# Kernel optimization log

Hardware: AMD Instinct MI355X
Metric: run time of the kernel (lower is better)

## Reference

```python
import jax, jax.numpy as jnp
import numpy as np

N = 8192
IN_F = 256
HEADS = 4
HF = 64            # head_features = out_features / heads
OUT_F = HEADS * HF # concat=True
NEG_SLOPE = 0.2


def setup_inputs() -> dict:
    key = jax.random.key(0)
    ks = jax.random.split(key, 7)
    x = jax.random.normal(ks[0], (N, IN_F), dtype=jnp.float32)
    graph = jax.random.randint(ks[1], (N, N), 0, 2, dtype=jnp.int32)
    weight = jax.random.normal(ks[2], (HEADS, IN_F, HF), dtype=jnp.float32) * (1.0 / np.sqrt(IN_F))
    weight_i = jax.random.normal(ks[3], (HEADS, HF, 1), dtype=jnp.float32) * (1.0 / np.sqrt(HF))
    weight_j = jax.random.normal(ks[4], (HEADS, HF, 1), dtype=jnp.float32) * (1.0 / np.sqrt(HF))
    weight_r = jax.random.normal(ks[5], (IN_F, HF * HEADS), dtype=jnp.float32) * (1.0 / np.sqrt(IN_F))
    bias = jnp.zeros((OUT_F,), dtype=jnp.float32)
    return {"x": x, "graph": graph, "weight": weight, "weight_i": weight_i,
            "weight_j": weight_j, "weight_r": weight_r, "bias": bias}


def reference(x, graph, weight, weight_i, weight_j, weight_r, bias):
    # h: per-head projected features [heads, N, hf]
    h = jnp.einsum('nm,hmf->hnf', x, weight)
    # additive attention logits: coe_i [h,N,1] + coe_j [h,1,N]
    coe_i = jnp.einsum('hnf,hfo->hno', h, weight_i)          # [heads, N, 1]
    coe_j = jnp.einsum('hnf,hfo->hno', h, weight_j)          # [heads, N, 1]
    coe = jax.nn.leaky_relu(coe_i + jnp.swapaxes(coe_j, 1, 2), NEG_SLOPE)  # [heads, N, N]
    # adjacency mask (note transpose, matching the torch code)
    mask = jnp.where(graph > 0, 0.0, -jnp.inf).T             # [N, N]
    att = jax.nn.softmax(coe + mask[None], axis=-1)          # [heads, N, N]
    # aggregate and move heads to axis 1: [N, heads, hf]
    y = jnp.einsum('hij,hjf->ihf', att, h)
    # residual with projection (in_features != head_features)
    y = y + (x @ weight_r).reshape(N, HEADS, HF)
    # concat heads + bias
    y = y.reshape(N, OUT_F) + bias
    return y
```

## Files before the change

kernel.cpp:

```cpp
#include <hip/hip_runtime.h>
#include <hip/hip_bf16.h>

#define N 8192
#define IN_F 256
#define HEADS 4
#define HF 64
#define OUT_F 256

typedef __attribute__((ext_vector_type(8))) short short8;
typedef __attribute__((ext_vector_type(4))) float f32x4;

__device__ __forceinline__ float lrelu(float x) {
    return fmaxf(x, 0.0f) * 0.8f + x * 0.2f;
}
__device__ __forceinline__ short f2bf(float f) {
    union { __hip_bfloat16 h; short s; } u;
    u.h = __float2bfloat16(f);
    return u.s;
}
__device__ __forceinline__ float bf2f(unsigned short b) {
    union { unsigned u; float f; } v; v.u = ((unsigned)b) << 16;
    return v.f;
}
__device__ __forceinline__ unsigned pack_bf16(float p0, float p1) {
    union { __hip_bfloat162 b; unsigned u; } cv;
    cv.b = __float22bfloat162_rn(make_float2(p0, p1));
    return cv.u;
}

__global__ __launch_bounds__(256) void k_wcvt(
    const float* __restrict__ w, const float* __restrict__ wr,
    unsigned short* __restrict__ BbT)
{
    int c = blockIdx.x;
    int k = threadIdx.x;
    float v;
    if (c < 256) {
        int head = c >> 6, f = c & 63;
        v = w[((size_t)head * IN_F + k) * HF + f];
    } else {
        v = wr[(size_t)k * OUT_F + (c - 256)];
    }
    BbT[(size_t)c * IN_F + k] = (unsigned short)f2bf(v);
}

__global__ __launch_bounds__(256) void k_gemm_pack(
    const float* __restrict__ x, const unsigned short* __restrict__ BbT,
    const float* __restrict__ bias,
    unsigned short* __restrict__ hT, float* __restrict__ out,
    const int* __restrict__ graph, unsigned int* __restrict__ bits)
{
    __shared__ unsigned short Asw[64 * 64];
    __shared__ unsigned short Bsw[128 * 64];
    int b = blockIdx.x;
    int t = threadIdx.x;

    if (b >= 512) {
        int p = b - 512;
        int jw = p & 255;
        int i = (p >> 8) * 256 + t;
        const int* gp = graph + (size_t)(jw * 32) * N + i;
        unsigned int word = 0;
        #pragma unroll
        for (int k = 0; k < 32; ++k)
            word |= (gp[(size_t)k * N] > 0 ? 1u : 0u) << k;
        bits[(size_t)jw * N + i] = word;
        return;
    }

    int m0 = (b & 127) * 64;
    int bn = b >> 7;
    int w_ = t >> 6, l = t & 63;
    int wr_ = w_ >> 1, wc_ = w_ & 1;
    int ar = l & 15, g = l >> 4;

    f32x4 acc[2][4];
    #pragma unroll
    for (int m = 0; m < 2; ++m)
        #pragma unroll
        for (int n = 0; n < 4; ++n) acc[m][n] = (f32x4){0.f, 0.f, 0.f, 0.f};

    int srow = t >> 2, skq = (t & 3) * 16;
    int sc = t >> 1, sh = (t & 1) * 32;

    for (int kt = 0; kt < 4; ++kt) {
        const float* xs = x + (size_t)(m0 + srow) * IN_F + kt * 64 + skq;
        float4 xa = ((const float4*)xs)[0];
        float4 xb = ((const float4*)xs)[1];
        float4 xc = ((const float4*)xs)[2];
        float4 xd = ((const float4*)xs)[3];
        unsigned ae[8];
        ae[0] = pack_bf16(xa.x, xa.y); ae[1] = pack_bf16(xa.z, xa.w);
        ae[2] = pack_bf16(xb.x, xb.y); ae[3] = pack_bf16(xb.z, xb.w);
        ae[4] = pack_bf16(xc.x, xc.y); ae[5] = pack_bf16(xc.z, xc.w);
        ae[6] = pack_bf16(xd.x, xd.y); ae[7] = pack_bf16(xd.z, xd.w);
        int kb0 = (skq >> 3) ^ (srow & 7);
        int kb1 = ((skq >> 3) + 1) ^ (srow & 7);
        *(uint4*)&Asw[srow * 64 + kb0 * 8] = *(uint4*)&ae[0];
        *(uint4*)&Asw[srow * 64 + kb1 * 8] = *(uint4*)&ae[4];
        const unsigned short* bs = BbT + (size_t)(bn * 128 + sc) * IN_F + kt * 64 + sh;
        uint4 b0 = ((const uint4*)bs)[0];
        uint4 b1 = ((const uint4*)bs)[1];
        uint4 b2 = ((const uint4*)bs)[2];
        uint4 b3 = ((const uint4*)bs)[3];
        int hb = sh >> 3;
        *(uint4*)&Bsw[sc * 64 + ((hb + 0) ^ (sc & 7)) * 8] = b0;
        *(uint4*)&Bsw[sc * 64 + ((hb + 1) ^ (sc & 7)) * 8] = b1;
        *(uint4*)&Bsw[sc * 64 + ((hb + 2) ^ (sc & 7)) * 8] = b2;
        *(uint4*)&Bsw[sc * 64 + ((hb + 3) ^ (sc & 7)) * 8] = b3;
        __syncthreads();
        #pragma unroll
        for (int ks = 0; ks < 2; ++ks) {
            short8 af[2], bf[4];
            #pragma unroll
            for (int m = 0; m < 2; ++m) {
                int row = wr_ * 32 + m * 16 + ar;
                int kb = (ks * 4 + g) ^ (row & 7);
                af[m] = *(const short8*)&Asw[row * 64 + kb * 8];
            }
            #pragma unroll
            for (int n = 0; n < 4; ++n) {
                int c = wc_ * 64 + n * 16 + ar;
                int kb = (ks * 4 + g) ^ (c & 7);
                bf[n] = *(const short8*)&Bsw[c * 64 + kb * 8];
            }
            #pragma unroll
            for (int m = 0; m < 2; ++m)
                #pragma unroll
                for (int n = 0; n < 4; ++n)
                    acc[m][n] = __builtin_amdgcn_mfma_f32_16x16x32_bf16(af[m], bf[n], acc[m][n], 0, 0, 0);
        }
        __syncthreads();
    }
    #pragma unroll
    for (int m = 0; m < 2; ++m) {
        #pragma unroll
        for (int n = 0; n < 4; ++n) {
            int cg = bn * 128 + wc_ * 64 + n * 16 + ar;
            int mg0 = m0 + wr_ * 32 + m * 16 + g * 4;
            if (cg < 256) {
                int head = cg >> 6, f = cg & 63;
                unsigned pk[2];
                pk[0] = pack_bf16(acc[m][n][0], acc[m][n][1]);
                pk[1] = pack_bf16(acc[m][n][2], acc[m][n][3]);
                *(uint2*)(hT + (size_t)(head * HF + f) * N + mg0) = *(uint2*)pk;
            } else {
                float bb = bias[cg - 256];
                #pragma unroll
                for (int r = 0; r < 4; ++r)
                    out[(size_t)(mg0 + r) * OUT_F + (cg - 256)] = acc[m][n][r] + bb;
            }
        }
    }
}

__global__ __launch_bounds__(256) void k_coe(
    const unsigned short* __restrict__ hT, const float* __restrict__ wi,
    const float* __restrict__ wj, float* __restrict__ coe_i, float* __restrict__ coe_j)
{
    int head = blockIdx.y;
    int n = blockIdx.x * 256 + threadIdx.x;
    const unsigned short* hp = hT + (size_t)head * HF * N + n;
    float si = 0.f, sj = 0.f;
    #pragma unroll 8
    for (int f = 0; f < HF; ++f) {
        float hv = bf2f(hp[(size_t)f * N]);
        si = fmaf(hv, wi[head * HF + f], si);
        sj = fmaf(hv, wj[head * HF + f], sj);
    }
    coe_i[head * N + n] = si;
    coe_j[head * N + n] = sj;
}

__global__ __launch_bounds__(256) void k_cols(
    const float* __restrict__ coe_j, float* __restrict__ maxB,
    float* __restrict__ F, float* __restrict__ H)
{
    __shared__ float red[256];
    int head = blockIdx.x;
    int t = threadIdx.x;
    float m = -1e30f;
    for (int n = t; n < N; n += 256) {
        float b = coe_j[head * N + n];
        F[head * N + n] = __expf(b);
        H[head * N + n] = __expf(0.2f * b);
        m = fmaxf(m, b);
    }
    red[t] = m;
    __syncthreads();
    for (int s = 128; s > 0; s >>= 1) {
        if (t < s) red[t] = fmaxf(red[t], red[t + s]);
        __syncthreads();
    }
    if (t == 0) maxB[head] = red[0];
}

__device__ __forceinline__ short8 makeP(
    const float4& fa, const float4& fb4, const float4& ha, const float4& hb4,
    unsigned int mk, float Ei, float Gi)
{
    float fv[8] = {fa.x, fa.y, fa.z, fa.w, fb4.x, fb4.y, fb4.z, fb4.w};
    float hv[8] = {ha.x, ha.y, ha.z, ha.w, hb4.x, hb4.y, hb4.z, hb4.w};
    union { short8 s8; unsigned u[4]; } A;
    #pragma unroll
    for (int jp = 0; jp < 4; ++jp) {
        float p0 = fmaxf(Ei * fv[2 * jp],     Gi * hv[2 * jp]);
        float p1 = fmaxf(Ei * fv[2 * jp + 1], Gi * hv[2 * jp + 1]);
        int s0 = __builtin_amdgcn_sbfe((int)mk, 2 * jp, 1);
        int s1 = __builtin_amdgcn_sbfe((int)mk, 2 * jp + 1, 1);
        p0 = __int_as_float(__float_as_int(p0) & s0);
        p1 = __int_as_float(__float_as_int(p1) & s1);
        A.u[jp] = pack_bf16(p0, p1);
    }
    return A.s8;
}

__global__ __launch_bounds__(512) void k_att(
    const unsigned short* __restrict__ hT, const float* __restrict__ coe_i,
    const float* __restrict__ maxB, const float* __restrict__ F,
    const float* __restrict__ H, const unsigned int* __restrict__ bits,
    float* __restrict__ out)
{
    __shared__ char smem[65536];
    unsigned short* hb = (unsigned short*)smem;
    float* mbuf = (float*)smem;

    int t = threadIdx.x;
    int head = blockIdx.y;
    int i0 = blockIdx.x * 64;
    int w = t >> 6, l = t & 63;
    int rg = w >> 2, grp = w & 3;
    int ar = l & 15, g = l >> 4, g8 = g * 8;

    int irow0 = i0 + rg * 32 + ar;
    int irow1 = irow0 + 16;
    float mB = maxB[head];
    float a0 = coe_i[head * N + irow0];
    float a1 = coe_i[head * N + irow1];
    float M0 = lrelu(a0 + mB);
    float M1 = lrelu(a1 + mB);
    float Ei0 = __expf(a0 - M0), Gi0 = __expf(0.2f * a0 - M0);
    float Ei1 = __expf(a1 - M1), Gi1 = __expf(0.2f * a1 - M1);

    f32x4 acc0[4], acc1[4];
    #pragma unroll
    for (int fb = 0; fb < 4; ++fb) {
        acc0[fb] = (f32x4){0.f, 0.f, 0.f, 0.f};
        acc1[fb] = (f32x4){0.f, 0.f, 0.f, 0.f};
    }
    f32x4 accd0 = (f32x4){0.f, 0.f, 0.f, 0.f};
    f32x4 accd1 = (f32x4){0.f, 0.f, 0.f, 0.f};

    short8 ones;
    #pragma unroll
    for (int k = 0; k < 8; ++k) ones[k] = (short)0x3F80;

    int grp_s = t >> 7;
    int v = t & 127;
    int sf = v >> 1;
    int gsel = v & 1;
    const unsigned short* hsrc = hT + ((size_t)(head * HF + sf) * N) + grp_s * 64 + gsel * 32;
    int sfk = sf & 7;
    int wbase = grp_s * 4096 + sf * 64;
    int pgA = ((gsel * 4 + 0) ^ sfk) * 8;
    int pgB = ((gsel * 4 + 1) ^ sfk) * 8;
    int pgC = ((gsel * 4 + 2) ^ sfk) * 8;
    int pgD = ((gsel * 4 + 3) ^ sfk) * 8;

    const float* Fp = F + head * N + g8;
    const float* Hp = H + head * N + g8;
    const unsigned int* bp0 = bits + irow0;
    const unsigned int* bp1 = bits + irow1;

    uint4 hv0 = *(const uint4*)(hsrc + 0);
    uint4 hv1 = *(const uint4*)(hsrc + 8);
    uint4 hv2 = *(const uint4*)(hsrc + 16);
    uint4 hv3 = *(const uint4*)(hsrc + 24);
    int jt0 = grp * 64;
    size_t jw0 = (size_t)(jt0 >> 5);
    unsigned int mk00 = bp0[jw0 * N] >> g8;
    unsigned int mk01 = bp0[(jw0 + 1) * N] >> g8;
    unsigned int mk10 = bp1[jw0 * N] >> g8;
    unsigned int mk11 = bp1[(jw0 + 1) * N] >> g8;

    for (int s = 0; s < 32; ++s) {
        int jt = s * 256 + grp * 64;
        float4 fa0 = *(const float4*)(Fp + jt);
        float4 fb0 = *(const float4*)(Fp + jt + 4);
        float4 ha0 = *(const float4*)(Hp + jt);
        float4 hb0 = *(const float4*)(Hp + jt + 4);
        float4 fa1 = *(const float4*)(Fp + jt + 32);
        float4 fb1 = *(const float4*)(Fp + jt + 36);
        float4 ha1 = *(const float4*)(Hp + jt + 32);
        float4 hb1 = *(const float4*)(Hp + jt + 36);
        int bo = (s & 1) * 16384;
        *(uint4*)&hb[bo + wbase + pgA] = hv0;
        *(uint4*)&hb[bo + wbase + pgB] = hv1;
        *(uint4*)&hb[bo + wbase + pgC] = hv2;
        *(uint4*)&hb[bo + wbase + pgD] = hv3;
        int sn = (s + 1 < 32) ? s + 1 : s;
        const unsigned short* hn = hsrc + (size_t)sn * 256;
        hv0 = *(const uint4*)(hn + 0);
        hv1 = *(const uint4*)(hn + 8);
        hv2 = *(const uint4*)(hn + 16);
        hv3 = *(const uint4*)(hn + 24);
        int jtn = sn * 256 + grp * 64;
        size_t jwn = (size_t)(jtn >> 5);
        unsigned int nk00 = bp0[jwn * N] >> g8;
        unsigned int nk01 = bp0[(jwn + 1) * N] >> g8;
        unsigned int nk10 = bp1[jwn * N] >> g8;
        unsigned int nk11 = bp1[(jwn + 1) * N] >> g8;
        short8 af00 = makeP(fa0, fb0, ha0, hb0, mk00, Ei0, Gi0);
        short8 af10 = makeP(fa0, fb0, ha0, hb0, mk10, Ei1, Gi1);
        short8 af01 = makeP(fa1, fb1, ha1, hb1, mk01, Ei0, Gi0);
        short8 af11 = makeP(fa1, fb1, ha1, hb1, mk11, Ei1, Gi1);
        asm volatile("s_waitcnt lgkmcnt(0)" ::: "memory");
        __builtin_amdgcn_s_barrier();
        __builtin_amdgcn_sched_barrier(0);
        const unsigned short* rb = &hb[bo + grp * 4096];
        #pragma unroll
        for (int ss = 0; ss < 2; ++ss) {
            short8 a0f = ss ? af01 : af00;
            short8 a1f = ss ? af11 : af10;
            #pragma unroll
            for (int fb = 0; fb < 4; ++fb) {
                int row = fb * 16 + ar;
                int pg = (ss * 4 + g) ^ (ar & 7);
                short8 bfr = *(const short8*)&rb[row * 64 + pg * 8];
                acc0[fb] = __builtin_amdgcn_mfma_f32_16x16x32_bf16(a0f, bfr, acc0[fb], 0, 0, 0);
                acc1[fb] = __builtin_amdgcn_mfma_f32_16x16x32_bf16(a1f, bfr, acc1[fb], 0, 0, 0);
            }
            accd0 = __builtin_amdgcn_mfma_f32_16x16x32_bf16(a0f, ones, accd0, 0, 0, 0);
            accd1 = __builtin_amdgcn_mfma_f32_16x16x32_bf16(a1f, ones, accd1, 0, 0, 0);
        }
        mk00 = nk00; mk01 = nk01; mk10 = nk10; mk11 = nk11;
    }

    __syncthreads();
    int slot = rg * 64 + l;
    if (grp > 0) {
        float* dst = mbuf + (size_t)(grp - 1) * 5248 + slot * 41;
        #pragma unroll
        for (int fb = 0; fb < 4; ++fb)
            #pragma unroll
            for (int r = 0; r < 4; ++r) {
                dst[fb * 4 + r] = acc0[fb][r];
                dst[16 + fb * 4 + r] = acc1[fb][r];
            }
        #pragma unroll
        for (int r = 0; r < 4; ++r) {
            dst[32 + r] = accd0[r];
            dst[36 + r] = accd1[r];
        }
    }
    __syncthreads();
    if (grp == 0) {
        #pragma unroll
        for (int q = 0; q < 3; ++q) {
            const float* src = mbuf + (size_t)q * 5248 + slot * 41;
            #pragma unroll
            for (int fb = 0; fb < 4; ++fb)
                #pragma unroll
                for (int r = 0; r < 4; ++r) {
                    acc0[fb][r] += src[fb * 4 + r];
                    acc1[fb][r] += src[16 + fb * 4 + r];
                }
            #pragma unroll
            for (int r = 0; r < 4; ++r) {
                accd0[r] += src[32 + r];
                accd1[r] += src[36 + r];
            }
        }
        #pragma unroll
        for (int r = 0; r < 4; ++r) {
            float inv0 = 1.0f / accd0[r];
            float inv1 = 1.0f / accd1[r];
            int orow0 = i0 + rg * 32 + g * 4 + r;
            float* op0 = out + (size_t)orow0 * OUT_F + head * HF + ar;
            float* op1 = op0 + 16 * OUT_F;
            #pragma unroll
            for (int fb = 0; fb < 4; ++fb) {
                op0[fb * 16] += acc0[fb][r] * inv0;
                op1[fb * 16] += acc1[fb][r] * inv1;
            }
        }
    }
}

extern "C" void kernel_launch(void* const* d_in, const int* in_sizes, int n_in,
                              void* d_out, int out_size, void* d_ws, size_t ws_size,
                              hipStream_t stream) {
    const float* x     = (const float*)d_in[0];
    const int*   graph = (const int*)d_in[1];
    const float* w     = (const float*)d_in[2];
    const float* wi    = (const float*)d_in[3];
    const float* wj    = (const float*)d_in[4];
    const float* wr    = (const float*)d_in[5];
    const float* bias  = (const float*)d_in[6];
    float* out = (float*)d_out;

    char* ws = (char*)d_ws;
    unsigned short* hT  = (unsigned short*)(ws);
    float* coe_i = (float*)(ws + 4194304);
    float* coe_j = (float*)(ws + 4325376);
    float* maxB  = (float*)(ws + 4456448);
    float* F     = (float*)(ws + 4457472);
    float* H     = (float*)(ws + 4588544);
    unsigned short* BbT = (unsigned short*)(ws + 4719616);
    unsigned int* bits  = (unsigned int*)(ws + 4981760);

    k_wcvt<<<dim3(512), 256, 0, stream>>>(w, wr, BbT);
    k_gemm_pack<<<dim3(512 + 8192), 256, 0, stream>>>(x, BbT, bias, hT, out, graph, bits);
    k_coe<<<dim3(32, 4), 256, 0, stream>>>(hT, wi, wj, coe_i, coe_j);
    k_cols<<<dim3(4), 256, 0, stream>>>(coe_j, maxB, F, H);
    k_att<<<dim3(N / 64, HEADS), 512, 0, stream>>>(hT, coe_i, maxB, F, H, bits, out);
}
```

Measured before the change: 174.7 us.

## Stream hT tiles into LDS with direct global_load_lds double-buffering

Replaces the register-staged copy of the transposed h tile (global load into VGPRs, then ds_write with an XOR swizzle) with direct global-to-LDS 16-byte loads. The next tile is issued right after the barrier into the other buffer. The mask-bit prefetch is dropped, so mask words are now loaded in the same iteration they are used. This saves VGPRs and LDS write instructions, but it relies on __syncthreads to cover completion of the asynchronous LDS loads, and the mask loads are no longer prefetched.

```diff
diff --git a/kernel.cpp b/kernel.cpp
--- a/kernel.cpp
+++ b/kernel.cpp
@@ -27,6 +27,11 @@
     cv.b = __float22bfloat162_rn(make_float2(p0, p1));
     return cv.u;
 }
+
+#define GLOAD_LDS(gsrc, ldst) \
+    __builtin_amdgcn_global_load_lds( \
+        (const __attribute__((address_space(1))) void*)(gsrc), \
+        (__attribute__((address_space(3))) void*)(ldst), 16, 0, 0)
 
 __global__ __launch_bounds__(256) void k_wcvt(
     const float* __restrict__ w, const float* __restrict__ wr,
@@ -255,36 +260,35 @@
     #pragma unroll
     for (int k = 0; k < 8; ++k) ones[k] = (short)0x3F80;
 
-    int grp_s = t >> 7;
-    int v = t & 127;
-    int sf = v >> 1;
-    int gsel = v & 1;
-    const unsigned short* hsrc = hT + ((size_t)(head * HF + sf) * N) + grp_s * 64 + gsel * 32;
-    int sfk = sf & 7;
-    int wbase = grp_s * 4096 + sf * 64;
-    int pgA = ((gsel * 4 + 0) ^ sfk) * 8;
-    int pgB = ((gsel * 4 + 1) ^ sfk) * 8;
-    int pgC = ((gsel * 4 + 2) ^ sfk) * 8;
-    int pgD = ((gsel * 4 + 3) ^ sfk) * 8;
+    int tg = w >> 1;
+    int rb0 = (w & 1) * 32;
+    int lrow = l >> 3;
+    int slot = l & 7;
+    int gg = slot ^ lrow;
+    const unsigned short* qsrc[4];
+    #pragma unroll
+    for (int q = 0; q < 4; ++q) {
+        int sf = rb0 + q * 8 + lrow;
+        qsrc[q] = hT + (size_t)(head * HF + sf) * N + tg * 64 + gg * 8;
+    }
+    int ldsoff0 = tg * 4096 + rb0 * 64;
 
     const float* Fp = F + head * N + g8;
     const float* Hp = H + head * N + g8;
     const unsigned int* bp0 = bits + irow0;
     const unsigned int* bp1 = bits + irow1;
 
-    uint4 hv0 = *(const uint4*)(hsrc + 0);
-    uint4 hv1 = *(const uint4*)(hsrc + 8);
-    uint4 hv2 = *(const uint4*)(hsrc + 16);
-    uint4 hv3 = *(const uint4*)(hsrc + 24);
-    int jt0 = grp * 64;
-    size_t jw0 = (size_t)(jt0 >> 5);
-    unsigned int mk00 = bp0[jw0 * N] >> g8;
-    unsigned int mk01 = bp0[(jw0 + 1) * N] >> g8;
-    unsigned int mk10 = bp1[jw0 * N] >> g8;
-    unsigned int mk11 = bp1[(jw0 + 1) * N] >> g8;
+    #pragma unroll
+    for (int q = 0; q < 4; ++q)
+        GLOAD_LDS(qsrc[q], hb + ldsoff0 + q * 512);
 
     for (int s = 0; s < 32; ++s) {
         int jt = s * 256 + grp * 64;
+        size_t jwd = (size_t)(jt >> 5);
+        unsigned int mk00 = bp0[jwd * N] >> g8;
+        unsigned int mk01 = bp0[(jwd + 1) * N] >> g8;
+        unsigned int mk10 = bp1[jwd * N] >> g8;
+        unsigned int mk11 = bp1[(jwd + 1) * N] >> g8;
         float4 fa0 = *(const float4*)(Fp + jt);
         float4 fb0 = *(const float4*)(Fp + jt + 4);
         float4 ha0 = *(const float4*)(Hp + jt);
@@ -293,31 +297,23 @@
         float4 fb1 = *(const float4*)(Fp + jt + 36);
         float4 ha1 = *(const float4*)(Hp + jt + 32);
         float4 hb1 = *(const float4*)(Hp + jt + 36);
-        int bo = (s & 1) * 16384;
-        *(uint4*)&hb[bo + wbase + pgA] = hv0;
-        *(uint4*)&hb[bo + wbase + pgB] = hv1;
-        *(uint4*)&hb[bo + wbase + pgC] = hv2;
-        *(uint4*)&hb[bo + wbase + pgD] = hv3;
-        int sn = (s + 1 < 32) ? s + 1 : s;
-        const unsigned short* hn = hsrc + (size_t)sn * 256;
-        hv0 = *(const uint4*)(hn + 0);
-        hv1 = *(const uint4*)(hn + 8);
-        hv2 = *(const uint4*)(hn + 16);
-        hv3 = *(const uint4*)(hn + 24);
-        int jtn = sn * 256 + grp * 64;
-        size_t jwn = (size_t)(jtn >> 5);
-        unsigned int nk00 = bp0[jwn * N] >> g8;
-        unsigned int nk01 = bp0[(jwn + 1) * N] >> g8;
-        unsigned int nk10 = bp1[jwn * N] >> g8;
-        unsigned int nk11 = bp1[(jwn + 1) * N] >> g8;
         short8 af00 = makeP(fa0, fb0, ha0, hb0, mk00, Ei0, Gi0);
         short8 af10 = makeP(fa0, fb0, ha0, hb0, mk10, Ei1, Gi1);
         short8 af01 = makeP(fa1, fb1, ha1, hb1, mk01, Ei0, Gi0);
         short8 af11 = makeP(fa1, fb1, ha1, hb1, mk11, Ei1, Gi1);
-        asm volatile("s_waitcnt lgkmcnt(0)" ::: "memory");
-        __builtin_amdgcn_s_barrier();
-        __builtin_amdgcn_sched_barrier(0);
-        const unsigned short* rb = &hb[bo + grp * 4096];
+
+        __syncthreads();
+
+        if (s < 31) {
+            int bon = ((s + 1) & 1) * 16384;
+            int jn = (s + 1) * 256;
+            #pragma unroll
+            for (int q = 0; q < 4; ++q)
+                GLOAD_LDS(qsrc[q] + jn, hb + bon + ldsoff0 + q * 512);
+        }
+
+        int bo = (s & 1) * 16384;
+        const unsigned short* rbuf = &hb[bo + grp * 4096];
         #pragma unroll
         for (int ss = 0; ss < 2; ++ss) {
             short8 a0f = ss ? af01 : af00;
@@ -326,20 +322,19 @@
             for (int fb = 0; fb < 4; ++fb) {
                 int row = fb * 16 + ar;
                 int pg = (ss * 4 + g) ^ (ar & 7);
-                short8 bfr = *(const short8*)&rb[row * 64 + pg * 8];
+                short8 bfr = *(const short8*)&rbuf[row * 64 + pg * 8];
                 acc0[fb] = __builtin_amdgcn_mfma_f32_16x16x32_bf16(a0f, bfr, acc0[fb], 0, 0, 0);
                 acc1[fb] = __builtin_amdgcn_mfma_f32_16x16x32_bf16(a1f, bfr, acc1[fb], 0, 0, 0);
             }
             accd0 = __builtin_amdgcn_mfma_f32_16x16x32_bf16(a0f, ones, accd0, 0, 0, 0);
             accd1 = __builtin_amdgcn_mfma_f32_16x16x32_bf16(a1f, ones, accd1, 0, 0, 0);
         }
-        mk00 = nk00; mk01 = nk01; mk10 = nk10; mk11 = nk11;
     }
 
     __syncthreads();
-    int slot = rg * 64 + l;
+    int slot_m = rg * 64 + l;
     if (grp > 0) {
-        float* dst = mbuf + (size_t)(grp - 1) * 5248 + slot * 41;
+        float* dst = mbuf + (size_t)(grp - 1) * 5248 + slot_m * 41;
         #pragma unroll
         for (int fb = 0; fb < 4; ++fb)
             #pragma unroll
@@ -357,7 +352,7 @@
     if (grp == 0) {
         #pragma unroll
         for (int q = 0; q < 3; ++q) {
-            const float* src = mbuf + (size_t)q * 5248 + slot * 41;
+            const float* src = mbuf + (size_t)q * 5248 + slot_m * 41;
             #pragma unroll
             for (int fb = 0; fb < 4; ++fb)
                 #pragma unroll
```

Result: faster. 164.0 us (-6.1%).
